# Kernel tuning notes

Hardware: AMD Instinct MI355X
Metric: run time of the kernel (lower is better)

Reference implementation:

```python
import jax, jax.numpy as jnp
import numpy as np

THRESH = 0.7  # similarity_threshold from __init__
EPS = 1e-8    # torch cosine_similarity eps


def setup_inputs() -> dict:
    key = jax.random.key(0)
    ks = jax.random.split(key, 7)
    B, D, F, H, M, NMEM = 65536, 512, 10, 512, 256, 1024
    return {
        "query_features": jax.random.normal(ks[0], (B, D), jnp.float32),
        "B_mat": jax.random.normal(ks[1], (D, F), jnp.float32),
        "W1": jax.random.normal(ks[2], (2 * F, H), jnp.float32) * 0.05,
        "b1": jax.random.normal(ks[3], (H,), jnp.float32) * 0.01,
        "W2": jax.random.normal(ks[4], (H, M), jnp.float32) * 0.05,
        "b2": jax.random.normal(ks[5], (M,), jnp.float32) * 0.01,
        "memory_bank": jax.random.normal(ks[6], (NMEM, M), jnp.float32),
    }


def reference(query_features, B_mat, W1, b1, W2, b2, memory_bank):
    # Fourier features (eq. 8): [B, 2F]
    xp = query_features @ B_mat
    ff = jnp.concatenate([jnp.sin(xp), jnp.cos(xp)], axis=-1)
    # memory_net MLP -> query vectors [B, M]
    h = jax.nn.relu(ff @ W1 + b1)
    q = h @ W2 + b2
    # cosine similarity q vs memory bank (torch semantics: dot / max(|a||b|, eps))
    qn = jnp.linalg.norm(q, axis=-1, keepdims=True)          # [B,1]
    mn = jnp.linalg.norm(memory_bank, axis=-1, keepdims=True)  # [N,1]
    sim = (q @ memory_bank.T) / jnp.maximum(qn * mn.T, EPS)   # [B,N]
    max_sim = jnp.max(sim, axis=1)                            # [B]
    max_idx = jnp.argmax(sim, axis=1)                         # [B]
    relevant = memory_bank[max_idx]                           # [B,M] gather
    relevant = jnp.where((max_sim < THRESH)[:, None], 0.0, relevant)
    return relevant
```

## Files before the change

### kernel.cpp

```cpp
#include <hip/hip_runtime.h>
#include <hip/hip_bf16.h>


typedef __attribute__((ext_vector_type(8))) short short8;
typedef __attribute__((ext_vector_type(4))) float f32x4;

#define MFMA(a, b, c) __builtin_amdgcn_mfma_f32_16x16x32_bf16((a), (b), (c), 0, 0, 0)

static __device__ __forceinline__ short bfb(float f) {
  return (short)__builtin_bit_cast(unsigned short, __float2bfloat16(f));
}
static __device__ __forceinline__ unsigned short bf16bits(float f) {
  return __builtin_bit_cast(unsigned short, __float2bfloat16(f));
}
static __device__ __forceinline__ float sel10(const float a[10], int i) {
  float v = a[0];
#pragma unroll
  for (int j = 1; j < 10; ++j) v = (i == j) ? a[j] : v;
  return v;
}

typedef const __attribute__((address_space(1))) unsigned int* gas_p;
typedef __attribute__((address_space(3))) unsigned int* las_p;
static __device__ __forceinline__ void async16(const void* g, void* l) {
  __builtin_amdgcn_global_load_lds((gas_p)g, (las_p)l, 16, 0, 0);
}

__global__ __launch_bounds__(256) void prep_kernel(
    const float* __restrict__ W1, const float* __restrict__ W2,
    const float* __restrict__ mem, __hip_bfloat16* __restrict__ W1p,
    __hip_bfloat16* __restrict__ W2p, __hip_bfloat16* __restrict__ Mp) {
  const int b = blockIdx.x, tid = threadIdx.x;
  if (b < 16) {
    __shared__ float invl[64];
    const int w = tid >> 6, lane = tid & 63, g = lane >> 4, jj = lane & 15;
    {
      int r = w * 16 + jj;
      const float4* m4 = (const float4*)(mem + (size_t)(b * 64 + r) * 256);
      float ss = 0.f;
      for (int t = 0; t < 16; ++t) {
        float4 v = m4[g * 16 + t];
        ss += v.x * v.x + v.y * v.y + v.z * v.z + v.w * v.w;
      }
      ss += __shfl_xor(ss, 16);
      ss += __shfl_xor(ss, 32);
      if (g == 0) invl[r] = rsqrtf(fmaxf(ss, 1e-30f));
    }
    __syncthreads();
    for (int u = 0; u < 64; ++u) {
      int t = u * 256 + tid;
      int j = t & 7, lane2 = (t >> 3) & 63, kt = (t >> 9) & 7, nl = t >> 12;
      int g2 = lane2 >> 4, jp = lane2 & 15;
      int nloc = nl * 16 + jp;
      int kap = 32 * kt + 16 * (j >> 2) + 4 * g2 + (j & 3);
      float v = mem[(size_t)(b * 64 + nloc) * 256 + kap] * invl[nloc];
      Mp[(size_t)b * 16384 + t] = __float2bfloat16(v);
    }
  } else if (b == 16) {
    for (int idx = tid; idx < 16384; idx += 256) {
      int j = idx & 7, lane2 = (idx >> 3) & 63, ct = idx >> 9;
      int g2 = lane2 >> 4, jp = lane2 & 15;
      int k = 8 * g2 + j;
      float v = (k < 20) ? W1[k * 512 + ct * 16 + jp] : 0.f;
      W1p[idx] = __float2bfloat16(v);
    }
  } else {
    int bb = b - 17;
    for (int u = 0; u < 32; ++u) {
      int idx = bb * 8192 + u * 256 + tid;
      int j = idx & 7, lane2 = (idx >> 3) & 63, c = (idx >> 9) & 15, kt = idx >> 13;
      int g2 = lane2 >> 4, jp = lane2 & 15;
      int kap = 32 * kt + 16 * (j >> 2) + 4 * g2 + (j & 3);
      W2p[idx] = __float2bfloat16(W2[(size_t)kap * 256 + c * 16 + jp]);
    }
  }
}

__global__ __launch_bounds__(256) void ff_kernel(
    const float* __restrict__ query, const float* __restrict__ Bmat,
    __hip_bfloat16* __restrict__ ff) {
  __shared__ __align__(16) float Bl[10 * 512];
  for (int i = threadIdx.x; i < 5120; i += 256) {
    int d = i / 10, f = i - d * 10;
    Bl[f * 512 + d] = Bmat[i];
  }
  __syncthreads();
  const int wv = threadIdx.x >> 6, lane = threadIdx.x & 63;
  const int g = lane >> 4, jj = lane & 15;
  const long row = (long)blockIdx.x * 16 + wv * 4 + g;
  const float4* q4 = (const float4*)(query + row * 512);

  float acc[10];
#pragma unroll
  for (int f = 0; f < 10; ++f) acc[f] = 0.f;
#pragma unroll
  for (int k = 0; k < 8; ++k) {
    float4 qv = q4[jj + 16 * k];
#pragma unroll
    for (int f = 0; f < 10; ++f) {
      float4 bv = *(const float4*)(Bl + f * 512 + 4 * (jj + 16 * k));
      acc[f] = fmaf(qv.x, bv.x, fmaf(qv.y, bv.y, fmaf(qv.z, bv.z, fmaf(qv.w, bv.w, acc[f]))));
    }
  }
#pragma unroll
  for (int f = 0; f < 10; ++f) {
    float s = acc[f];
    s += __shfl_xor(s, 1); s += __shfl_xor(s, 2);
    s += __shfl_xor(s, 4); s += __shfl_xor(s, 8);
    acc[f] = s;
  }
  int base = (jj < 5) ? 2 * jj : 2 * jj - 10;
  float a0 = sel10(acc, base);
  float a1 = sel10(acc, base + 1);
  float v0 = 0.f, v1 = 0.f;
  if (jj < 5) { v0 = sinf(a0); v1 = sinf(a1); }
  else if (jj < 10) { v0 = cosf(a0); v1 = cosf(a1); }
  ushort2 pk;
  pk.x = bf16bits(v0);
  pk.y = bf16bits(v1);
  ((ushort2*)ff)[row * 16 + jj] = pk;
}

#define STAGE_W2(slab, bufi)                                             \
  do {                                                                   \
    const char* s_ = (const char*)W2p + (slab)*16384 + tid * 16;         \
    char* d_ = lds + (bufi)*16384 + tid * 16;                            \
    async16(s_, d_);                                                     \
    async16(s_ + 8192, d_ + 8192);                                       \
  } while (0)

#define STAGE_MP(slab, bufi)                                             \
  do {                                                                   \
    const char* s_ = (const char*)Mp + (slab)*32768 + tid * 16;          \
    char* d_ = lds + 32768 + (bufi)*32768 + tid * 16;                    \
    async16(s_, d_);                                                     \
    async16(s_ + 8192, d_ + 8192);                                       \
    async16(s_ + 16384, d_ + 16384);                                     \
    async16(s_ + 24576, d_ + 24576);                                     \
  } while (0)

__global__ __launch_bounds__(512, 2) void mega_kernel(
    const __hip_bfloat16* __restrict__ ff, const __hip_bfloat16* __restrict__ W1p,
    const float* __restrict__ b1, const __hip_bfloat16* __restrict__ W2p,
    const float* __restrict__ b2, const __hip_bfloat16* __restrict__ Mp,
    const float* __restrict__ mem, float* __restrict__ out) {
  __shared__ __align__(16) char lds[98304];
  const int tid = threadIdx.x, w = tid >> 6, lane = tid & 63;
  const int g = lane >> 4, jj = lane & 15;
  const int rowBase = blockIdx.x * 256 + w * 32;
  const f32x4 z4 = {0.f, 0.f, 0.f, 0.f};
  const short8* w1f = (const short8*)W1p;

  STAGE_W2(0, 0);

  short8 ffq[2];
#pragma unroll
  for (int rt = 0; rt < 2; ++rt)
    ffq[rt] = *(const short8*)(ff + (size_t)(rowBase + rt * 16 + jj) * 32 + g * 8);

  f32x4 acc3[2][16];
#pragma unroll
  for (int rt = 0; rt < 2; ++rt)
#pragma unroll
    for (int c = 0; c < 16; ++c) acc3[rt][c] = z4;

  short8 w1c0 = w1f[lane], w1c1 = w1f[64 + lane];

  __syncthreads();

  for (int t = 0; t < 16; ++t) {
    if (t < 15) STAGE_W2(t + 1, (t + 1) & 1);
    else STAGE_MP(0, 0);
    short8 w1n0 = w1c0, w1n1 = w1c1;
    if (t < 15) {
      w1n0 = w1f[(2 * t + 2) * 64 + lane];
      w1n1 = w1f[(2 * t + 3) * 64 + lane];
    }
    const char* buf = lds + (t & 1) * 16384;
    short8 hf[2];
#pragma unroll
    for (int half = 0; half < 2; ++half) {
      const int ct = 2 * t + half;
      f32x4 bb = *(const f32x4*)(b1 + ct * 16 + 4 * g);
      short8 a = half ? w1c1 : w1c0;
#pragma unroll
      for (int rt = 0; rt < 2; ++rt) {
        f32x4 d = MFMA(a, ffq[rt], z4);
#pragma unroll
        for (int i = 0; i < 4; ++i) {
          float v = d[i] + bb[i];
          v = v > 0.f ? v : 0.f;
          hf[rt][half * 4 + i] = bfb(v);
        }
      }
    }
#pragma unroll
    for (int c = 0; c < 16; ++c) {
      short8 bfr = *(const short8*)(buf + c * 1024 + lane * 16);
#pragma unroll
      for (int rt = 0; rt < 2; ++rt)
        acc3[rt][c] = MFMA(bfr, hf[rt], acc3[rt][c]);
    }
    w1c0 = w1n0;
    w1c1 = w1n1;
    __syncthreads();
  }

  short8 qfrag[2][8];
  float invqn[2];
#pragma unroll
  for (int rt = 0; rt < 2; ++rt) {
    float qn = 0.f;
#pragma unroll
    for (int c = 0; c < 16; ++c) {
      f32x4 bb = *(const f32x4*)(b2 + c * 16 + 4 * g);
#pragma unroll
      for (int i = 0; i < 4; ++i) {
        float v = acc3[rt][c][i] + bb[i];
        qn += v * v;
        qfrag[rt][c >> 1][(c & 1) * 4 + i] = bfb(v);
      }
    }
    qn += __shfl_xor(qn, 16);
    qn += __shfl_xor(qn, 32);
    invqn[rt] = rsqrtf(fmaxf(qn, 1e-30f));
  }

  float runmax[2][4];
  int runidx[2][4];
#pragma unroll
  for (int rt = 0; rt < 2; ++rt)
#pragma unroll
    for (int i = 0; i < 4; ++i) { runmax[rt][i] = -1e30f; runidx[rt][i] = 0; }

  for (int t = 0; t < 16; ++t) {
    if (t < 15) STAGE_MP(t + 1, (t + 1) & 1);
    const char* buf = lds + 32768 + (t & 1) * 32768;
    f32x4 a4[2][4];
#pragma unroll
    for (int rt = 0; rt < 2; ++rt)
#pragma unroll
      for (int nl = 0; nl < 4; ++nl) a4[rt][nl] = z4;
#pragma unroll
    for (int kt = 0; kt < 8; ++kt) {
#pragma unroll
      for (int nl = 0; nl < 4; ++nl) {
        short8 bfr = *(const short8*)(buf + (nl * 8 + kt) * 1024 + lane * 16);
#pragma unroll
        for (int rt = 0; rt < 2; ++rt)
          a4[rt][nl] = MFMA(qfrag[rt][kt], bfr, a4[rt][nl]);
      }
    }
#pragma unroll
    for (int nl = 0; nl < 4; ++nl) {
      int n = (t * 4 + nl) * 16 + jj;
#pragma unroll
      for (int rt = 0; rt < 2; ++rt)
#pragma unroll
        for (int i = 0; i < 4; ++i) {
          if (a4[rt][nl][i] > runmax[rt][i]) {
            runmax[rt][i] = a4[rt][nl][i];
            runidx[rt][i] = n;
          }
        }
    }
    __syncthreads();
  }

  const float4* mem4 = (const float4*)mem;
  float4* out4 = (float4*)out;
#pragma unroll
  for (int rt = 0; rt < 2; ++rt) {
#pragma unroll
    for (int i = 0; i < 4; ++i) {
#pragma unroll
      for (int o = 1; o < 16; o <<= 1) {
        float v2 = __shfl_xor(runmax[rt][i], o);
        int i2 = __shfl_xor(runidx[rt][i], o);
        if (v2 > runmax[rt][i] || (v2 == runmax[rt][i] && i2 < runidx[rt][i])) {
          runmax[rt][i] = v2;
          runidx[rt][i] = i2;
        }
      }
    }
#pragma unroll
    for (int i = 0; i < 4; ++i) {
      float iq = __shfl(invqn[rt], 4 * g + i, 64);
      float ms = runmax[rt][i] * iq;
      int s = (ms < 0.7f) ? -1 : runidx[rt][i];
      size_t row = (size_t)rowBase + rt * 16 + 4 * g + i;
#pragma unroll
      for (int cq = 0; cq < 4; ++cq) {
        int col = cq * 16 + jj;
        float4 v = {0.f, 0.f, 0.f, 0.f};
        if (s >= 0) v = mem4[(size_t)s * 64 + col];
        out4[row * 64 + col] = v;
      }
    }
  }
}

extern "C" void kernel_launch(void* const* d_in, const int* in_sizes, int n_in,
                              void* d_out, int out_size, void* d_ws, size_t ws_size,
                              hipStream_t stream) {
  const float* query = (const float*)d_in[0];
  const float* Bmat = (const float*)d_in[1];
  const float* W1 = (const float*)d_in[2];
  const float* b1 = (const float*)d_in[3];
  const float* W2 = (const float*)d_in[4];
  const float* b2 = (const float*)d_in[5];
  const float* mem = (const float*)d_in[6];
  float* out = (float*)d_out;

  char* ws = (char*)d_ws;
  __hip_bfloat16* ff = (__hip_bfloat16*)ws;
  __hip_bfloat16* Mp = (__hip_bfloat16*)(ws + 4194304);
  __hip_bfloat16* W2p = (__hip_bfloat16*)(ws + 4194304 + 524288);
  __hip_bfloat16* W1p = (__hip_bfloat16*)(ws + 4194304 + 786432);

  prep_kernel<<<dim3(33), dim3(256), 0, stream>>>(W1, W2, mem, W1p, W2p, Mp);
  ff_kernel<<<dim3(4096), dim3(256), 0, stream>>>(query, Bmat, ff);
  mega_kernel<<<dim3(256), dim3(512), 0, stream>>>(ff, W1p, b1, W2p, b2, Mp, mem, out);
}
```

Before: 117.2 us.

## Merge prep and ff kernels; halve mega block size and staging slabs

Merges the weight/memory-bank prep kernel and the Fourier-feature kernel into one launch, with ff blocks each handling two rows per thread group. The main kernel moves to 256-thread blocks covering 128 rows, 512 blocks in all, with 64KB LDS and memory-bank slabs of half the size over 32 iterations. The goal is to cut a launch, spread work over more CUs and raise occupancy through lower LDS use. The cost is more barrier iterations, and each block now restages W2 and the whole memory bank, doubling that global traffic.

Result: faster. 101.0 us (-13.8%).

```diff
diff --git a/kernel.cpp b/kernel.cpp
--- a/kernel.cpp
+++ b/kernel.cpp
@@ -26,13 +26,16 @@
   __builtin_amdgcn_global_load_lds((gas_p)g, (las_p)l, 16, 0, 0);
 }
 
-__global__ __launch_bounds__(256) void prep_kernel(
+__global__ __launch_bounds__(256) void prep_ff_kernel(
     const float* __restrict__ W1, const float* __restrict__ W2,
-    const float* __restrict__ mem, __hip_bfloat16* __restrict__ W1p,
-    __hip_bfloat16* __restrict__ W2p, __hip_bfloat16* __restrict__ Mp) {
+    const float* __restrict__ mem, const float* __restrict__ query,
+    const float* __restrict__ Bmat, __hip_bfloat16* __restrict__ W1p,
+    __hip_bfloat16* __restrict__ W2p, __hip_bfloat16* __restrict__ Mp,
+    __hip_bfloat16* __restrict__ ff) {
+  __shared__ __align__(16) float Bl[10 * 512];
   const int b = blockIdx.x, tid = threadIdx.x;
   if (b < 16) {
-    __shared__ float invl[64];
+    float* invl = Bl;
     const int w = tid >> 6, lane = tid & 63, g = lane >> 4, jj = lane & 15;
     {
       int r = w * 16 + jj;
@@ -64,7 +67,7 @@
       float v = (k < 20) ? W1[k * 512 + ct * 16 + jp] : 0.f;
       W1p[idx] = __float2bfloat16(v);
     }
-  } else {
+  } else if (b < 33) {
     int bb = b - 17;
     for (int u = 0; u < 32; ++u) {
       int idx = bb * 8192 + u * 256 + tid;
@@ -73,81 +76,85 @@
       int kap = 32 * kt + 16 * (j >> 2) + 4 * g2 + (j & 3);
       W2p[idx] = __float2bfloat16(W2[(size_t)kap * 256 + c * 16 + jp]);
     }
-  }
-}
-
-__global__ __launch_bounds__(256) void ff_kernel(
-    const float* __restrict__ query, const float* __restrict__ Bmat,
-    __hip_bfloat16* __restrict__ ff) {
-  __shared__ __align__(16) float Bl[10 * 512];
-  for (int i = threadIdx.x; i < 5120; i += 256) {
-    int d = i / 10, f = i - d * 10;
-    Bl[f * 512 + d] = Bmat[i];
-  }
-  __syncthreads();
-  const int wv = threadIdx.x >> 6, lane = threadIdx.x & 63;
-  const int g = lane >> 4, jj = lane & 15;
-  const long row = (long)blockIdx.x * 16 + wv * 4 + g;
-  const float4* q4 = (const float4*)(query + row * 512);
-
-  float acc[10];
-#pragma unroll
-  for (int f = 0; f < 10; ++f) acc[f] = 0.f;
-#pragma unroll
-  for (int k = 0; k < 8; ++k) {
-    float4 qv = q4[jj + 16 * k];
-#pragma unroll
-    for (int f = 0; f < 10; ++f) {
-      float4 bv = *(const float4*)(Bl + f * 512 + 4 * (jj + 16 * k));
-      acc[f] = fmaf(qv.x, bv.x, fmaf(qv.y, bv.y, fmaf(qv.z, bv.z, fmaf(qv.w, bv.w, acc[f]))));
-    }
-  }
-#pragma unroll
-  for (int f = 0; f < 10; ++f) {
-    float s = acc[f];
-    s += __shfl_xor(s, 1); s += __shfl_xor(s, 2);
-    s += __shfl_xor(s, 4); s += __shfl_xor(s, 8);
-    acc[f] = s;
-  }
-  int base = (jj < 5) ? 2 * jj : 2 * jj - 10;
-  float a0 = sel10(acc, base);
-  float a1 = sel10(acc, base + 1);
-  float v0 = 0.f, v1 = 0.f;
-  if (jj < 5) { v0 = sinf(a0); v1 = sinf(a1); }
-  else if (jj < 10) { v0 = cosf(a0); v1 = cosf(a1); }
-  ushort2 pk;
-  pk.x = bf16bits(v0);
-  pk.y = bf16bits(v1);
-  ((ushort2*)ff)[row * 16 + jj] = pk;
-}
-
-#define STAGE_W2(slab, bufi)                                             \
-  do {                                                                   \
-    const char* s_ = (const char*)W2p + (slab)*16384 + tid * 16;         \
-    char* d_ = lds + (bufi)*16384 + tid * 16;                            \
-    async16(s_, d_);                                                     \
-    async16(s_ + 8192, d_ + 8192);                                       \
+  } else {
+    const int bb = b - 33;
+    for (int i = tid; i < 5120; i += 256) {
+      int d = i / 10, f = i - d * 10;
+      Bl[f * 512 + d] = Bmat[i];
+    }
+    __syncthreads();
+    const int wv = tid >> 6, lane = tid & 63;
+    const int g = lane >> 4, jj = lane & 15;
+    const long r0 = (long)bb * 32 + (wv * 4 + g) * 2;
+    const float4* qa = (const float4*)(query + r0 * 512);
+    const float4* qb = (const float4*)(query + (r0 + 1) * 512);
+
+    float acc[2][10];
+#pragma unroll
+    for (int f = 0; f < 10; ++f) { acc[0][f] = 0.f; acc[1][f] = 0.f; }
+#pragma unroll
+    for (int k = 0; k < 8; ++k) {
+      float4 va = qa[jj + 16 * k];
+      float4 vb = qb[jj + 16 * k];
+#pragma unroll
+      for (int f = 0; f < 10; ++f) {
+        float4 bv = *(const float4*)(Bl + f * 512 + 4 * (jj + 16 * k));
+        acc[0][f] = fmaf(va.x, bv.x, fmaf(va.y, bv.y, fmaf(va.z, bv.z, fmaf(va.w, bv.w, acc[0][f]))));
+        acc[1][f] = fmaf(vb.x, bv.x, fmaf(vb.y, bv.y, fmaf(vb.z, bv.z, fmaf(vb.w, bv.w, acc[1][f]))));
+      }
+    }
+#pragma unroll
+    for (int r = 0; r < 2; ++r) {
+#pragma unroll
+      for (int f = 0; f < 10; ++f) {
+        float s = acc[r][f];
+        s += __shfl_xor(s, 1); s += __shfl_xor(s, 2);
+        s += __shfl_xor(s, 4); s += __shfl_xor(s, 8);
+        acc[r][f] = s;
+      }
+      int base = (jj < 5) ? 2 * jj : 2 * jj - 10;
+      float a0 = sel10(acc[r], base);
+      float a1 = sel10(acc[r], base + 1);
+      float v0 = 0.f, v1 = 0.f;
+      if (jj < 5) { v0 = sinf(a0); v1 = sinf(a1); }
+      else if (jj < 10) { v0 = cosf(a0); v1 = cosf(a1); }
+      ushort2 pk;
+      pk.x = bf16bits(v0);
+      pk.y = bf16bits(v1);
+      ((ushort2*)ff)[(r0 + r) * 16 + jj] = pk;
+    }
+  }
+}
+
+#define STAGE_W2(slab, bufi)                                      \
+  do {                                                            \
+    const char* s_ = (const char*)W2p + (slab)*16384 + tid * 16;  \
+    char* d_ = lds + (bufi)*16384 + tid * 16;                     \
+    async16(s_, d_);                                              \
+    async16(s_ + 4096, d_ + 4096);                                \
+    async16(s_ + 8192, d_ + 8192);                                \
+    async16(s_ + 12288, d_ + 12288);                              \
   } while (0)
 
-#define STAGE_MP(slab, bufi)                                             \
-  do {                                                                   \
-    const char* s_ = (const char*)Mp + (slab)*32768 + tid * 16;          \
-    char* d_ = lds + 32768 + (bufi)*32768 + tid * 16;                    \
-    async16(s_, d_);                                                     \
-    async16(s_ + 8192, d_ + 8192);                                       \
-    async16(s_ + 16384, d_ + 16384);                                     \
-    async16(s_ + 24576, d_ + 24576);                                     \
+#define STAGE_MP(slab, bufi)                                      \
+  do {                                                            \
+    const char* s_ = (const char*)Mp + (slab)*16384 + tid * 16;   \
+    char* d_ = lds + 32768 + (bufi)*16384 + tid * 16;             \
+    async16(s_, d_);                                              \
+    async16(s_ + 4096, d_ + 4096);                                \
+    async16(s_ + 8192, d_ + 8192);                                \
+    async16(s_ + 12288, d_ + 12288);                              \
   } while (0)
 
-__global__ __launch_bounds__(512, 2) void mega_kernel(
+__global__ __launch_bounds__(256, 2) void mega_kernel(
     const __hip_bfloat16* __restrict__ ff, const __hip_bfloat16* __restrict__ W1p,
     const float* __restrict__ b1, const __hip_bfloat16* __restrict__ W2p,
     const float* __restrict__ b2, const __hip_bfloat16* __restrict__ Mp,
     const float* __restrict__ mem, float* __restrict__ out) {
-  __shared__ __align__(16) char lds[98304];
+  __shared__ __align__(16) char lds[65536];
   const int tid = threadIdx.x, w = tid >> 6, lane = tid & 63;
   const int g = lane >> 4, jj = lane & 15;
-  const int rowBase = blockIdx.x * 256 + w * 32;
+  const int rowBase = blockIdx.x * 128 + w * 32;
   const f32x4 z4 = {0.f, 0.f, 0.f, 0.f};
   const short8* w1f = (const short8*)W1p;
 
@@ -233,18 +240,18 @@
 #pragma unroll
     for (int i = 0; i < 4; ++i) { runmax[rt][i] = -1e30f; runidx[rt][i] = 0; }
 
-  for (int t = 0; t < 16; ++t) {
-    if (t < 15) STAGE_MP(t + 1, (t + 1) & 1);
-    const char* buf = lds + 32768 + (t & 1) * 32768;
-    f32x4 a4[2][4];
+  for (int t = 0; t < 32; ++t) {
+    if (t < 31) STAGE_MP(t + 1, (t + 1) & 1);
+    const char* buf = lds + 32768 + (t & 1) * 16384;
+    f32x4 a4[2][2];
 #pragma unroll
     for (int rt = 0; rt < 2; ++rt)
 #pragma unroll
-      for (int nl = 0; nl < 4; ++nl) a4[rt][nl] = z4;
+      for (int nl = 0; nl < 2; ++nl) a4[rt][nl] = z4;
 #pragma unroll
     for (int kt = 0; kt < 8; ++kt) {
 #pragma unroll
-      for (int nl = 0; nl < 4; ++nl) {
+      for (int nl = 0; nl < 2; ++nl) {
         short8 bfr = *(const short8*)(buf + (nl * 8 + kt) * 1024 + lane * 16);
 #pragma unroll
         for (int rt = 0; rt < 2; ++rt)
@@ -252,8 +259,8 @@
       }
     }
 #pragma unroll
-    for (int nl = 0; nl < 4; ++nl) {
-      int n = (t * 4 + nl) * 16 + jj;
+    for (int nl = 0; nl < 2; ++nl) {
+      int n = (t * 2 + nl) * 16 + jj;
 #pragma unroll
       for (int rt = 0; rt < 2; ++rt)
 #pragma unroll
@@ -318,7 +325,7 @@
   __hip_bfloat16* W2p = (__hip_bfloat16*)(ws + 4194304 + 524288);
   __hip_bfloat16* W1p = (__hip_bfloat16*)(ws + 4194304 + 786432);
 
-  prep_kernel<<<dim3(33), dim3(256), 0, stream>>>(W1, W2, mem, W1p, W2p, Mp);
-  ff_kernel<<<dim3(4096), dim3(256), 0, stream>>>(query, Bmat, ff);
-  mega_kernel<<<dim3(256), dim3(512), 0, stream>>>(ff, W1p, b1, W2p, b2, Mp, mem, out);
-}
+  prep_ff_kernel<<<dim3(2081), dim3(256), 0, stream>>>(W1, W2, mem, query, Bmat,
+                                                       W1p, W2p, Mp, ff);
+  mega_kernel<<<dim3(512), dim3(256), 0, stream>>>(ff, W1p, b1, W2p, b2, Mp, mem, out);
+}
```
